# Optimization experiments

Measured on AMD Instinct MI355X. Metric: run time of the kernel, lower is better.

## Reference

```python
import jax, jax.numpy as jnp
import numpy as np
from jax.scipy.special import logsumexp

EPSILON = 0.1
N_ITERS = 5


def setup_inputs() -> dict:
    key = jax.random.key(0)
    k1, k2, k3 = jax.random.split(key, 3)
    B, Q, T, D = 16, 1024, 1024, 256
    preds = jax.random.normal(k1, (B, Q, D), dtype=jnp.float32)
    targets = jax.random.normal(k2, (B, T, D), dtype=jnp.float32)
    filter = jax.random.normal(k3, (B, T), dtype=jnp.float32)
    return {"preds": preds, "targets": targets, "filter": filter}


def _cdist(x, y):
    x2 = jnp.sum(x * x, axis=-1)[:, :, None]          # [B,Q,1]
    y2 = jnp.sum(y * y, axis=-1)[:, None, :]          # [B,1,T]
    xy = jnp.einsum("bqd,btd->bqt", x, y)             # [B,Q,T]
    return jnp.sqrt(jnp.maximum(x2 + y2 - 2.0 * xy, 0.0))


def reference(preds, targets, filter):
    eps = EPSILON
    B, Q, _ = preds.shape
    T = targets.shape[1]
    cost = _cdist(preds, targets)                     # [B,Q,T]
    filter_cost = 2.0 * jnp.max(cost)
    cost = jnp.where(filter[:, None, :] <= 0, filter_cost, cost)
    u = jnp.zeros((B, Q), dtype=cost.dtype)
    v = jnp.zeros((B, T), dtype=cost.dtype)
    for _ in range(N_ITERS):
        u = -eps * logsumexp(-(cost - v[:, None, :]) / eps, axis=2)
        v = -eps * logsumexp(-(cost - u[:, :, None]) / eps, axis=1)
    P = jnp.exp((u[:, :, None] + v[:, None, :] - cost) / eps)
    idx_tgt = jnp.argmax(P, axis=2)
    return (idx_tgt, P)
```

## Files before the change

### kernel.cpp

```cpp
#include <hip/hip_runtime.h>
#include <math.h>

#define BB 16
#define QQ 1024
#define TT 1024
#define DD 256
#define EPS 0.1f
#define SINK_ITERS 5
#define FCONST 128.0f
#define K2 14.426950408889634f
#define EPSLN2 0.069314718055994531f

typedef _Float16 f16;
typedef _Float16 f16x4 __attribute__((ext_vector_type(4)));
typedef _Float16 f16x8 __attribute__((ext_vector_type(8)));
typedef float f32x4 __attribute__((ext_vector_type(4)));

__device__ __forceinline__ float fast_exp2(float x) {
#if __has_builtin(__builtin_amdgcn_exp2f)
  return __builtin_amdgcn_exp2f(x);
#else
  return exp2f(x);
#endif
}
__device__ __forceinline__ float fast_log2(float x) {
#if __has_builtin(__builtin_amdgcn_logf)
  return __builtin_amdgcn_logf(x);
#else
  return log2f(x);
#endif
}

__global__ __launch_bounds__(256) void cvt_kernel(
    const float* __restrict__ preds, const float* __restrict__ targets,
    f16* __restrict__ Ahi, f16* __restrict__ Alo,
    f16* __restrict__ Bhi, f16* __restrict__ Blo,
    float* __restrict__ x2, float* __restrict__ y2)
{
  int w = threadIdx.x >> 6, l = threadIdx.x & 63;
  int row = blockIdx.x * 4 + w;
  const float* src; f16 *hi, *lo; float* nrm;
  if (row < BB*QQ) {
    src = preds + (size_t)row * DD;
    hi = Ahi + (size_t)row * DD; lo = Alo + (size_t)row * DD; nrm = x2 + row;
  } else {
    int r = row - BB*QQ;
    src = targets + (size_t)r * DD;
    hi = Bhi + (size_t)r * DD; lo = Blo + (size_t)r * DD; nrm = y2 + r;
  }
  float4 v = ((const float4*)src)[l];
  f16x4 h, lw;
  h.x = (f16)v.x; h.y = (f16)v.y; h.z = (f16)v.z; h.w = (f16)v.w;
  lw.x = (f16)(v.x - (float)h.x); lw.y = (f16)(v.y - (float)h.y);
  lw.z = (f16)(v.z - (float)h.z); lw.w = (f16)(v.w - (float)h.w);
  *(f16x4*)(hi + l*4) = h;
  *(f16x4*)(lo + l*4) = lw;
  float s = v.x*v.x + v.y*v.y + v.z*v.z + v.w*v.w;
  #pragma unroll
  for (int o = 32; o; o >>= 1) s += __shfl_down(s, o, 64);
  if (l == 0) *nrm = s;
}

__global__ __launch_bounds__(256) void scan_kernel(
    const float* __restrict__ filter, int* __restrict__ nU,
    int* __restrict__ f0i, int* __restrict__ cidx)
{
  __shared__ int sc[256];
  __shared__ int sf0;
  int b = blockIdx.x, tid = threadIdx.x;
  if (tid == 0) sf0 = 0x7fffffff;
  __syncthreads();
  float4 f4 = ((const float4*)(filter + (size_t)b*TT))[tid];
  int i0 = f4.x > 0.f, i1 = f4.y > 0.f, i2 = f4.z > 0.f, i3 = f4.w > 0.f;
  int cnt = i0+i1+i2+i3;
  int t0 = tid*4;
// ... 8 lines not shown
    sc[tid] += val;
    __syncthreads();
  }
  int excl = sc[tid] - cnt;
  int* cb = cidx + (size_t)b*TT + t0;
  int run = excl;
  cb[0] = run; run += i0;
  cb[1] = run; run += i1;
  cb[2] = run; run += i2;
  cb[3] = run; run += i3;
  if (tid == 255) nU[b] = sc[255];
  __syncthreads();
  if (tid == 0) f0i[b] = sf0;
}

__global__ __launch_bounds__(256) void cost_mfma_kernel(
    const f16* __restrict__ Ahi, const f16* __restrict__ Alo,
    const f16* __restrict__ Bhi, const f16* __restrict__ Blo,
    const float* __restrict__ x2, const float* __restrict__ y2,
    const float* __restrict__ filter,
    float* __restrict__ cost, float* __restrict__ costT, int useT,
    float* __restrict__ costC, const int* __restrict__ cidx, int compact)
{
  __shared__ f16 sA[2][128*32];
  __shared__ f16 sB[2][128*32];
  int b = blockIdx.z;
  int q0 = blockIdx.y * 128, t0 = blockIdx.x * 128;
  int tid = threadIdx.x, w = tid >> 6, l = tid & 63;
  int rq = (w >> 1) * 64, rt = (w & 1) * 64;
  int fr = l & 15, fg = l >> 4;
  const f16* pA[2] = { Ahi + ((size_t)b*QQ + q0) * DD, Alo + ((size_t)b*QQ + q0) * DD };
  const f16* pB[2] = { Bhi + ((size_t)b*TT + t0) * DD, Blo + ((size_t)b*TT + t0) * DD };
  f32x4 acc[4][4] = {};
  for (int k0 = 0; k0 < DD; k0 += 32) {
    __syncthreads();
#if __has_builtin(__builtin_amdgcn_global_load_lds)
    #pragma unroll
    for (int j = 0; j < 2; ++j) {
      int chunk = w*128 + j*64 + l;
      int row = chunk >> 2, kc = chunk & 3;
      size_t go = (size_t)row * DD + k0 + kc*8;
      int lb = (w*128 + j*64) * 8;
// ... 34 lines not shown
    #pragma unroll
    for (int fm = 0; fm < 4; ++fm)
      #pragma unroll
      for (int fn = 0; fn < 4; ++fn) {
        acc[fm][fn] = __builtin_amdgcn_mfma_f32_16x16x32_f16(ah[fm], bh[fn], acc[fm][fn], 0, 0, 0);
        acc[fm][fn] = __builtin_amdgcn_mfma_f32_16x16x32_f16(ah[fm], bl[fn], acc[fm][fn], 0, 0, 0);
        acc[fm][fn] = __builtin_amdgcn_mfma_f32_16x16x32_f16(al[fm], bh[fn], acc[fm][fn], 0, 0, 0);
      }
  }
  float xv[16];
  #pragma unroll
  for (int fm = 0; fm < 4; ++fm)
    #pragma unroll
    for (int r = 0; r < 4; ++r)
      xv[fm*4+r] = x2[(size_t)b*QQ + q0 + rq + fm*16 + fg*4 + r];
  float yv[4], fv[4];
  int jn[4];
  #pragma unroll
  for (int fn = 0; fn < 4; ++fn) {
    int t = t0 + rt + fn*16 + fr;
    yv[fn] = y2[(size_t)b*TT + t];
    fv[fn] = filter[(size_t)b*TT + t];
    jn[fn] = compact ? cidx[(size_t)b*TT + t] : 0;
  }
  #pragma unroll
  for (int fm = 0; fm < 4; ++fm) {
    #pragma unroll
    for (int fn = 0; fn < 4; ++fn) {
      int t = t0 + rt + fn*16 + fr;
      float cvr[4];
      #pragma unroll
      for (int r = 0; r < 4; ++r) {
        float c2 = xv[fm*4+r] + yv[fn] - 2.0f*acc[fm][fn][r];
        float craw = sqrtf(fmaxf(c2, 0.f));
        cvr[r] = craw;
        int q = q0 + rq + fm*16 + fg*4 + r;
        if (!compact) {
          cost[((size_t)b*QQ + q)*TT + t] = (fv[fn] <= 0.f) ? FCONST : craw;
        } else if (fv[fn] > 0.f) {
          costC[((size_t)b*QQ + q)*TT + jn[fn]] = craw;
        }
      }
      if (useT && fv[fn] > 0.f) {
        float* dst = costT + ((size_t)b*TT + t)*QQ + q0 + rq + fm*16 + fg*4;
        *(float4*)dst = make_float4(cvr[0], cvr[1], cvr[2], cvr[3]);
      }
    }
  }
}

__global__ __launch_bounds__(64) void norms_kernel(
    const float* __restrict__ preds, const float* __restrict__ targets,
    float* __restrict__ x2, float* __restrict__ y2)
{
  int row = blockIdx.x;
  const float* src; float* dst;
  if (row < BB*QQ) { src = preds + (size_t)row * DD; dst = x2 + row; }
  else { int r = row - BB*QQ; src = targets + (size_t)r * DD; dst = y2 + r; }
  float4 v = ((const float4*)src)[threadIdx.x];
  float s = v.x*v.x + v.y*v.y + v.z*v.z + v.w*v.w;
  #pragma unroll
  for (int o = 32; o; o >>= 1) s += __shfl_down(s, o, 64);
  if (threadIdx.x == 0) *dst = s;
}

#define LDSTR 132
__global__ __launch_bounds__(256) void cost_fp32_kernel(
    const float* __restrict__ preds, const float* __restrict__ targets,
    const float* __restrict__ x2, const float* __restrict__ y2,
    const float* __restrict__ filter,
    float* __restrict__ cost, float* __restrict__ costT, int useT)
{
  __shared__ float As[16*LDSTR];
  __shared__ float Bs[16*LDSTR];
  int b  = blockIdx.z;
  int q0 = blockIdx.y * 128;
  int t0 = blockIdx.x * 128;
  const float* Ab = preds   + ((size_t)b*QQ + q0) * DD;
  const float* Bb = targets + ((size_t)b*TT + t0) * DD;
  int tid = threadIdx.x;
  int srow = tid >> 2, sq = (tid & 3) << 2;
  int w = tid >> 6, l = tid & 63;
  int rq = ((w >> 1) << 6) + ((l >> 3) << 3);
  int rt = ((w & 1) << 6) + ((l & 7) << 3);
  float acc[8][8] = {};
  for (int k0 = 0; k0 < DD; k0 += 16) {
// ... 38 lines not shown
  #pragma unroll
  for (int i = 0; i < 8; ++i)
    #pragma unroll
    for (int j = 0; j < 8; ++j) {
      float c2 = xq[i] + yt[j] - 2.f*acc[i][j];
      float c = sqrtf(fmaxf(c2, 0.f));
      if (fvv[j] <= 0.f) c = FCONST;
      cv[i][j] = c;
    }
  #pragma unroll
  for (int i = 0; i < 8; ++i) {
    float* dst = cost + ((size_t)b*QQ + q0 + rq + i) * TT + t0 + rt;
    *(float4*)dst       = make_float4(cv[i][0], cv[i][1], cv[i][2], cv[i][3]);
    *(float4*)(dst + 4) = make_float4(cv[i][4], cv[i][5], cv[i][6], cv[i][7]);
  }
  if (useT) {
    #pragma unroll
    for (int j = 0; j < 8; ++j) {
      if (fvv[j] <= 0.f) continue;
      float* dst = costT + ((size_t)b*TT + t0 + rt + j) * QQ + q0 + rq;
      *(float4*)dst       = make_float4(cv[0][j], cv[1][j], cv[2][j], cv[3][j]);
      *(float4*)(dst + 4) = make_float4(cv[4][j], cv[5][j], cv[6][j], cv[7][j]);
    }
  }
}

__device__ __forceinline__ float wave_max64(float v) {
  #pragma unroll
  for (int o = 1; o < 64; o <<= 1) v = fmaxf(v, __shfl_xor(v, o, 64));
  return v;
}
__device__ __forceinline__ float wave_sum64(float v) {
  #pragma unroll
  for (int o = 1; o < 64; o <<= 1) v += __shfl_xor(v, o, 64);
  return v;
}

__global__ __launch_bounds__(256) void u_c_kernel(
    const float* __restrict__ costC, const float* __restrict__ vC,
    const float* __restrict__ vf, const int* __restrict__ nU,
    float* __restrict__ u, int it0)
{
  int w = threadIdx.x >> 6, l = threadIdx.x & 63;
  int row = blockIdx.x * 8 + w * 2;
  int b = row >> 10;
  int n = nU[b];
  int nF = TT - n;
  const float4* c0 = (const float4*)(costC + (size_t)row * TT);
  const float4* c1 = c0 + TT/4;
  const float4* vb = (const float4*)(vC + (size_t)b * TT);
  float s0[16], s1[16], m0 = -3.0e38f, m1 = -3.0e38f;
  int iters = (n + 255) >> 8;
  #pragma unroll
  for (int i = 0; i < 4; ++i) {
    if (i < iters) {
      int jj = l + (i << 6);
      int j = jj << 2;
      float4 v4;
      if (it0) v4 = make_float4(0.f,0.f,0.f,0.f); else v4 = vb[jj];
      float4 a4 = c0[jj];
      float4 b4 = c1[jj];
      s0[4*i+0] = (j+0 < n) ? (v4.x - a4.x)*K2 : -3.0e38f;
      s0[4*i+1] = (j+1 < n) ? (v4.y - a4.y)*K2 : -3.0e38f;
      s0[4*i+2] = (j+2 < n) ? (v4.z - a4.z)*K2 : -3.0e38f;
      s0[4*i+3] = (j+3 < n) ? (v4.w - a4.w)*K2 : -3.0e38f;
      s1[4*i+0] = (j+0 < n) ? (v4.x - b4.x)*K2 : -3.0e38f;
      s1[4*i+1] = (j+1 < n) ? (v4.y - b4.y)*K2 : -3.0e38f;
      s1[4*i+2] = (j+2 < n) ? (v4.z - b4.z)*K2 : -3.0e38f;
      s1[4*i+3] = (j+3 < n) ? (v4.w - b4.w)*K2 : -3.0e38f;
      m0 = fmaxf(m0, fmaxf(fmaxf(s0[4*i+0], s0[4*i+1]), fmaxf(s0[4*i+2], s0[4*i+3])));
      m1 = fmaxf(m1, fmaxf(fmaxf(s1[4*i+0], s1[4*i+1]), fmaxf(s1[4*i+2], s1[4*i+3])));
    } else {
      #pragma unroll
      for (int k = 0; k < 4; ++k) { s0[4*i+k] = -3.0e38f; s1[4*i+k] = -3.0e38f; }
    }
  }
  float st = 0.f;
  if (nF > 0) {
    float vfb = it0 ? 0.f : vf[b];
    st = (vfb - FCONST) * K2;
    m0 = fmaxf(m0, st); m1 = fmaxf(m1, st);
  }
  m0 = wave_max64(m0); m1 = wave_max64(m1);
  float q0 = 0.f, q1 = 0.f;
  #pragma unroll
  for (int i = 0; i < 16; ++i) { q0 += fast_exp2(s0[i] - m0); q1 += fast_exp2(s1[i] - m1); }
  q0 = wave_sum64(q0); q1 = wave_sum64(q1);
  if (nF > 0) {
    q0 += (float)nF * fast_exp2(st - m0);
    q1 += (float)nF * fast_exp2(st - m1);
  }
  if (l == 0) {
    u[row]   = -EPSLN2 * (m0 + fast_log2(q0));
    u[row+1] = -EPSLN2 * (m1 + fast_log2(q1));
  }
}

__global__ __launch_bounds__(256) void v_c_kernel(
    const float* __restrict__ costT,
    const float* __restrict__ filter, const int* __restrict__ cidx,
    const float* __restrict__ u, float* __restrict__ v,
    float* __restrict__ vC, float* __restrict__ vf)
{
  int w = threadIdx.x >> 6, l = threadIdx.x & 63;
  int row = blockIdx.x * 8 + w * 2;
  int b = row >> 10;
  const float4* ub = (const float4*)(u + (size_t)b * QQ);
  bool f0 = (filter[row]   <= 0.f);
  bool f1 = (filter[row+1] <= 0.f);
  float4 uw[4];
  #pragma unroll
  for (int i = 0; i < 4; ++i) uw[i] = ub[l + (i << 6)];
  float s0[16], s1[16], m0 = -3.0e38f, m1 = -3.0e38f;
  if (f0) {
    #pragma unroll
    for (int i = 0; i < 4; ++i) {
      s0[4*i+0] = (uw[i].x - FCONST) * K2; s0[4*i+1] = (uw[i].y - FCONST) * K2;
      s0[4*i+2] = (uw[i].z - FCONST) * K2; s0[4*i+3] = (uw[i].w - FCONST) * K2;
    }
  } else {
    const float4* cr = (const float4*)(costT + (size_t)row * QQ);
    #pragma unroll
    for (int i = 0; i < 4; ++i) {
      float4 c4 = cr[l + (i << 6)];
      s0[4*i+0] = (uw[i].x - c4.x) * K2; s0[4*i+1] = (uw[i].y - c4.y) * K2;
      s0[4*i+2] = (uw[i].z - c4.z) * K2; s0[4*i+3] = (uw[i].w - c4.w) * K2;
    }
  }
  if (f1) {
    #pragma unroll
    for (int i = 0; i < 4; ++i) {
      s1[4*i+0] = (uw[i].x - FCONST) * K2; s1[4*i+1] = (uw[i].y - FCONST) * K2;
      s1[4*i+2] = (uw[i].z - FCONST) * K2; s1[4*i+3] = (uw[i].w - FCONST) * K2;
    }
  } else {
    const float4* cr = (const float4*)(costT + (size_t)(row+1) * QQ);
    #pragma unroll
    for (int i = 0; i < 4; ++i) {
      float4 c4 = cr[l + (i << 6)];
      s1[4*i+0] = (uw[i].x - c4.x) * K2; s1[4*i+1] = (uw[i].y - c4.y) * K2;
      s1[4*i+2] = (uw[i].z - c4.z) * K2; s1[4*i+3] = (uw[i].w - c4.w) * K2;
    }
  }
  #pragma unroll
  for (int i = 0; i < 16; ++i) { m0 = fmaxf(m0, s0[i]); m1 = fmaxf(m1, s1[i]); }
  m0 = wave_max64(m0); m1 = wave_max64(m1);
  float q0 = 0.f, q1 = 0.f;
  #pragma unroll
  for (int i = 0; i < 16; ++i) { q0 += fast_exp2(s0[i] - m0); q1 += fast_exp2(s1[i] - m1); }
  q0 = wave_sum64(q0); q1 = wave_sum64(q1);
  if (l == 0) {
    float val0 = -EPSLN2 * (m0 + fast_log2(q0));
    float val1 = -EPSLN2 * (m1 + fast_log2(q1));
    v[row]   = val0;
    v[row+1] = val1;
    if (f0) vf[b] = val0; else vC[(size_t)b*TT + cidx[row]] = val0;
    if (f1) vf[b] = val1; else vC[(size_t)b*TT + cidx[row+1]] = val1;
  }
}

__global__ __launch_bounds__(256) void p_c_kernel(
    const float* __restrict__ costC, const float* __restrict__ filter,
    const int* __restrict__ cidx, const int* __restrict__ nU,
    const int* __restrict__ f0i, const float* __restrict__ vf,
    const float* __restrict__ u, const float* __restrict__ v,
    float* __restrict__ P, float* __restrict__ idxOut)
{
  int w = threadIdx.x >> 6, l = threadIdx.x & 63;
  int row = blockIdx.x * 8 + w * 2;
  int b = row >> 10;
  int nF = TT - nU[b];
  float u0 = u[row], u1 = u[row+1];
  float pf0 = -1.f, pf1 = -1.f; int fidx = 0x7fffffff;
  if (nF > 0) {
    float vfb = vf[b];
    pf0 = fast_exp2((u0 + vfb - FCONST) * K2);
    pf1 = fast_exp2((u1 + vfb - FCONST) * K2);
    fidx = f0i[b];
  }
  const float* r0 = costC + (size_t)row * TT;
  const float* r1 = r0 + TT;
  float4* o0 = (float4*)(P + (size_t)row * TT);
  float4* o1 = o0 + TT/4;
  const float4* fb = (const float4*)(filter + (size_t)b * TT);
  const int4*   jb = (const int4*)(cidx + (size_t)b * TT);
  const float4* vv = (const float4*)(v + (size_t)b * TT);
  float bp0 = -1.f, bp1 = -1.f; int bt0 = 0x7ffffffe, bt1 = 0x7ffffffe;
  #pragma unroll
  for (int i = 0; i < 4; ++i) {
    int e = l + (i << 6);
    float4 f4 = fb[e];
    int4  j4 = jb[e];
    float4 v4 = vv[e];
    int tb = e << 2;
    float4 p0, p1;
#define PELEM(comp, jx, toff) \
    if (f4.comp > 0.f) { \
      float cA = r0[jx], cB = r1[jx]; \
      p0.comp = fast_exp2((u0 + v4.comp - cA) * K2); \
      p1.comp = fast_exp2((u1 + v4.comp - cB) * K2); \
      if (p0.comp > bp0) { bp0 = p0.comp; bt0 = tb + toff; } \
      if (p1.comp > bp1) { bp1 = p1.comp; bt1 = tb + toff; } \
    } else { p0.comp = pf0; p1.comp = pf1; }
    PELEM(x, j4.x, 0)
    PELEM(y, j4.y, 1)
    PELEM(z, j4.z, 2)
    PELEM(w, j4.w, 3)
#undef PELEM
    o0[e] = p0;
    o1[e] = p1;
  }
  #pragma unroll
  for (int o = 1; o < 64; o <<= 1) {
    float op = __shfl_xor(bp0, o, 64);
    int   ot = __shfl_xor(bt0, o, 64);
    if (op > bp0 || (op == bp0 && ot < bt0)) { bp0 = op; bt0 = ot; }
    op = __shfl_xor(bp1, o, 64);
    ot = __shfl_xor(bt1, o, 64);
    if (op > bp1 || (op == bp1 && ot < bt1)) { bp1 = op; bt1 = ot; }
  }
  if (l == 0) {
    if (pf0 > bp0 || (pf0 == bp0 && fidx < bt0)) bt0 = fidx;
    if (pf1 > bp1 || (pf1 == bp1 && fidx < bt1)) bt1 = fidx;
    idxOut[row]   = (float)bt0;
    idxOut[row+1] = (float)bt1;
  }
}

__device__ __forceinline__ void u_body(int row, int l, bool it0,
    const float* __restrict__ cost, const float* __restrict__ v, float* __restrict__ u)
{
  int b = row >> 10;
  const float4* c0 = (const float4*)(cost + (size_t)row * TT);
  const float4* c1 = c0 + TT/4;
  const float4* vb = (const float4*)(v + (size_t)b * TT);
  float s0[16], s1[16], m0 = -3.0e38f, m1 = -3.0e38f;
  #pragma unroll
  for (int i = 0; i < 4; ++i) {
    float4 v4;
    if (it0) v4 = make_float4(0.f, 0.f, 0.f, 0.f);
    else     v4 = vb[l + (i << 6)];
    float4 a4 = c0[l + (i << 6)];
    float4 b4 = c1[l + (i << 6)];
    s0[4*i+0] = (v4.x - a4.x) * K2; s0[4*i+1] = (v4.y - a4.y) * K2;
    s0[4*i+2] = (v4.z - a4.z) * K2; s0[4*i+3] = (v4.w - a4.w) * K2;
    s1[4*i+0] = (v4.x - b4.x) * K2; s1[4*i+1] = (v4.y - b4.y) * K2;
    s1[4*i+2] = (v4.z - b4.z) * K2; s1[4*i+3] = (v4.w - b4.w) * K2;
    m0 = fmaxf(m0, fmaxf(fmaxf(s0[4*i+0], s0[4*i+1]), fmaxf(s0[4*i+2], s0[4*i+3])));
    m1 = fmaxf(m1, fmaxf(fmaxf(s1[4*i+0], s1[4*i+1]), fmaxf(s1[4*i+2], s1[4*i+3])));
  }
  m0 = wave_max64(m0); m1 = wave_max64(m1);
  float q0 = 0.f, q1 = 0.f;
  #pragma unroll
  for (int i = 0; i < 16; ++i) { q0 += fast_exp2(s0[i] - m0); q1 += fast_exp2(s1[i] - m1); }
  q0 = wave_sum64(q0); q1 = wave_sum64(q1);
  if (l == 0) {
    u[row]   = -EPSLN2 * (m0 + fast_log2(q0));
    u[row+1] = -EPSLN2 * (m1 + fast_log2(q1));
  }
}

__global__ __launch_bounds__(256) void u_kernel(
    const float* __restrict__ cost, const float* __restrict__ v, float* __restrict__ u, int it0)
{
  u_body(blockIdx.x * 8 + (threadIdx.x >> 6) * 2, threadIdx.x & 63, it0 != 0, cost, v, u);
}

__global__ __launch_bounds__(256) void v_kernel(
    const float* __restrict__ cost, const float* __restrict__ costT, int useT,
    const float* __restrict__ filter, const float* __restrict__ u, float* __restrict__ v)
{
  int w = threadIdx.x >> 6, l = threadIdx.x & 63;
  int row = blockIdx.x * 8 + w * 2;
  int b = row >> 10, t = row & 1023;
  const float4* ub = (const float4*)(u + (size_t)b * QQ);
  bool f0 = (filter[row]   <= 0.f);
  bool f1 = (filter[row+1] <= 0.f);
  float4 uw[4];
  #pragma unroll
  for (int i = 0; i < 4; ++i) uw[i] = ub[l + (i << 6)];
  float s0[16], s1[16], m0 = -3.0e38f, m1 = -3.0e38f;
  if (f0) {
    #pragma unroll
    for (int i = 0; i < 4; ++i) {
      s0[4*i+0] = (uw[i].x - FCONST) * K2; s0[4*i+1] = (uw[i].y - FCONST) * K2;
      s0[4*i+2] = (uw[i].z - FCONST) * K2; s0[4*i+3] = (uw[i].w - FCONST) * K2;
    }
  } else if (useT) {
    const float4* cr = (const float4*)(costT + (size_t)row * QQ);
    #pragma unroll
    for (int i = 0; i < 4; ++i) {
      float4 c4 = cr[l + (i << 6)];
      s0[4*i+0] = (uw[i].x - c4.x) * K2; s0[4*i+1] = (uw[i].y - c4.y) * K2;
      s0[4*i+2] = (uw[i].z - c4.z) * K2; s0[4*i+3] = (uw[i].w - c4.w) * K2;
    }
  } else {
    const float* cr = cost + (size_t)b*QQ*TT + t;
    #pragma unroll
    for (int i = 0; i < 4; ++i) {
      int q = (l + (i << 6)) << 2;
      s0[4*i+0] = (uw[i].x - cr[(size_t)(q+0)*TT]) * K2;
      s0[4*i+1] = (uw[i].y - cr[(size_t)(q+1)*TT]) * K2;
      s0[4*i+2] = (uw[i].z - cr[(size_t)(q+2)*TT]) * K2;
      s0[4*i+3] = (uw[i].w - cr[(size_t)(q+3)*TT]) * K2;
    }
  }
  if (f1) {
    #pragma unroll
    for (int i = 0; i < 4; ++i) {
      s1[4*i+0] = (uw[i].x - FCONST) * K2; s1[4*i+1] = (uw[i].y - FCONST) * K2;
      s1[4*i+2] = (uw[i].z - FCONST) * K2; s1[4*i+3] = (uw[i].w - FCONST) * K2;
    }
  } else if (useT) {
    const float4* cr = (const float4*)(costT + (size_t)(row+1) * QQ);
    #pragma unroll
    for (int i = 0; i < 4; ++i) {
      float4 c4 = cr[l + (i << 6)];
      s1[4*i+0] = (uw[i].x - c4.x) * K2; s1[4*i+1] = (uw[i].y - c4.y) * K2;
      s1[4*i+2] = (uw[i].z - c4.z) * K2; s1[4*i+3] = (uw[i].w - c4.w) * K2;
    }
  } else {
    const float* cr = cost + (size_t)b*QQ*TT + t + 1;
    #pragma unroll
    for (int i = 0; i < 4; ++i) {
      int q = (l + (i << 6)) << 2;
      s1[4*i+0] = (uw[i].x - cr[(size_t)(q+0)*TT]) * K2;
      s1[4*i+1] = (uw[i].y - cr[(size_t)(q+1)*TT]) * K2;
      s1[4*i+2] = (uw[i].z - cr[(size_t)(q+2)*TT]) * K2;
      s1[4*i+3] = (uw[i].w - cr[(size_t)(q+3)*TT]) * K2;
    }
  }
  #pragma unroll
  for (int i = 0; i < 16; ++i) { m0 = fmaxf(m0, s0[i]); m1 = fmaxf(m1, s1[i]); }
  m0 = wave_max64(m0); m1 = wave_max64(m1);
  float q0 = 0.f, q1 = 0.f;
  #pragma unroll
  for (int i = 0; i < 16; ++i) { q0 += fast_exp2(s0[i] - m0); q1 += fast_exp2(s1[i] - m1); }
  q0 = wave_sum64(q0); q1 = wave_sum64(q1);
  if (l == 0) {
    v[row]   = -EPSLN2 * (m0 + fast_log2(q0));
    v[row+1] = -EPSLN2 * (m1 + fast_log2(q1));
  }
}

// ... 51 lines not shown
                              void* d_out, int out_size, void* d_ws, size_t ws_size,
                              hipStream_t stream) {
  const float* preds   = (const float*)d_in[0];
  const float* targets = (const float*)d_in[1];
  const float* filter  = (const float*)d_in[2];
  float* out = (float*)d_out;
  float* idxOut = out;
  float* P = out + (size_t)BB*QQ;

  const size_t F16A   = (size_t)BB*QQ*DD;
  const size_t f16tot = 4 * F16A * sizeof(f16);
  const size_t SMALL  = (size_t)1 << 19;
  const size_t CB     = (size_t)BB * QQ * TT * sizeof(float);

  char* ws = (char*)d_ws;
  int useF16 = ws_size >= f16tot + SMALL;
  char* base = ws + (useF16 ? f16tot : 0);
  f16 *Ahi = (f16*)ws, *Alo = Ahi + F16A, *Bhi = Alo + F16A, *Blo = Bhi + F16A;
  float* x2 = (float*)base;
  float* y2 = x2 + 16384;
  float* u  = y2 + 16384;
  float* v  = u + 16384;
  float* vC = v + 16384;
  float* vf = vC + 16384;
  int* nU   = (int*)(vf + 64);
  int* f0i  = nU + 64;
  int* cidx = f0i + 64;
  float* costT = (float*)(base + SMALL);
  float* costC = (float*)(base + SMALL + CB);
  int useT = ws_size >= (size_t)(base - ws) + SMALL + CB;
  int useC = useF16 && (ws_size >= f16tot + SMALL + 2*CB);

  dim3 cg_(TT/128, QQ/128, BB);
  if (useF16) {
    cvt_kernel<<<BB*(QQ+TT)/4, 256, 0, stream>>>(preds, targets, Ahi, Alo, Bhi, Blo, x2, y2);
    if (useC) scan_kernel<<<BB, 256, 0, stream>>>(filter, nU, f0i, cidx);
    cost_mfma_kernel<<<cg_, 256, 0, stream>>>(Ahi, Alo, Bhi, Blo, x2, y2, filter,
                                              P, costT, useT, costC, cidx, useC);
  } else {
    norms_kernel<<<BB*(QQ+TT), 64, 0, stream>>>(preds, targets, x2, y2);
    cost_fp32_kernel<<<cg_, 256, 0, stream>>>(preds, targets, x2, y2, filter, P, costT, useT);
  }

  int blks = BB*QQ/8;
  if (useC) {
    for (int it = 0; it < SINK_ITERS; ++it) {
      u_c_kernel<<<blks, 256, 0, stream>>>(costC, vC, vf, nU, u, it == 0 ? 1 : 0);
      v_c_kernel<<<blks, 256, 0, stream>>>(costT, filter, cidx, u, v, vC, vf);
    }
    p_c_kernel<<<blks, 256, 0, stream>>>(costC, filter, cidx, nU, f0i, vf, u, v, P, idxOut);
  } else {
    for (int it = 0; it < SINK_ITERS; ++it) {
      u_kernel<<<blks, 256, 0, stream>>>(P, v, u, it == 0 ? 1 : 0);
      v_kernel<<<blks, 256, 0, stream>>>(P, costT, useT, filter, u, v);
    }
    p_kernel<<<blks, 256, 0, stream>>>(P, u, v, idxOut);
  }
}
```

Before: 267.9 us.

## Compact unfiltered targets before GEMM and skip fully filtered column tiles

Runs the filter scan first, then has the conversion kernel write only unfiltered target rows, in compacted order, into the f16 B operand. The MFMA cost kernel now runs on these compacted targets and exits early for column tiles past the unfiltered count. It writes the compacted cost and its transpose directly, with no per-element filter checks or index gathers. About half the targets are filtered under random normal inputs, so roughly half the GEMM and cost stores should be skipped. Tiles that straddle the count boundary still compute some garbage columns, and the fallback paths are simplified.

```diff
diff --git a/kernel.cpp b/kernel.cpp
--- a/kernel.cpp
+++ b/kernel.cpp
@@ -29,36 +29,6 @@
 #else
   return log2f(x);
 #endif
-}
-
-__global__ __launch_bounds__(256) void cvt_kernel(
-    const float* __restrict__ preds, const float* __restrict__ targets,
-    f16* __restrict__ Ahi, f16* __restrict__ Alo,
-    f16* __restrict__ Bhi, f16* __restrict__ Blo,
-    float* __restrict__ x2, float* __restrict__ y2)
-{
-  int w = threadIdx.x >> 6, l = threadIdx.x & 63;
-  int row = blockIdx.x * 4 + w;
-  const float* src; f16 *hi, *lo; float* nrm;
-  if (row < BB*QQ) {
-    src = preds + (size_t)row * DD;
-    hi = Ahi + (size_t)row * DD; lo = Alo + (size_t)row * DD; nrm = x2 + row;
-  } else {
-    int r = row - BB*QQ;
-    src = targets + (size_t)r * DD;
-    hi = Bhi + (size_t)r * DD; lo = Blo + (size_t)r * DD; nrm = y2 + r;
-  }
-  float4 v = ((const float4*)src)[l];
-  f16x4 h, lw;
-  h.x = (f16)v.x; h.y = (f16)v.y; h.z = (f16)v.z; h.w = (f16)v.w;
-  lw.x = (f16)(v.x - (float)h.x); lw.y = (f16)(v.y - (float)h.y);
-  lw.z = (f16)(v.z - (float)h.z); lw.w = (f16)(v.w - (float)h.w);
-  *(f16x4*)(hi + l*4) = h;
-  *(f16x4*)(lo + l*4) = lw;
-  float s = v.x*v.x + v.y*v.y + v.z*v.z + v.w*v.w;
-  #pragma unroll
-  for (int o = 32; o; o >>= 1) s += __shfl_down(s, o, 64);
-  if (l == 0) *nrm = s;
 }
 
 __global__ __launch_bounds__(256) void scan_kernel(
@@ -97,18 +67,53 @@
   if (tid == 0) f0i[b] = sf0;
 }
 
-__global__ __launch_bounds__(256) void cost_mfma_kernel(
+__global__ __launch_bounds__(256) void cvt_c_kernel(
+    const float* __restrict__ preds, const float* __restrict__ targets,
+    const float* __restrict__ filter, const int* __restrict__ cidx,
+    f16* __restrict__ Ahi, f16* __restrict__ Alo,
+    f16* __restrict__ Bhi, f16* __restrict__ Blo,
+    float* __restrict__ x2, float* __restrict__ y2)
+{
+  int w = threadIdx.x >> 6, l = threadIdx.x & 63;
+  int row = blockIdx.x * 4 + w;
+  const float* src; f16 *hi, *lo; float* nrm;
+  if (row < BB*QQ) {
+    src = preds + (size_t)row * DD;
+    hi = Ahi + (size_t)row * DD; lo = Alo + (size_t)row * DD; nrm = x2 + row;
+  } else {
+    int r = row - BB*QQ;
+    if (filter[r] <= 0.f) return;
+    int b = r >> 10;
+    int cj = cidx[r];
+    size_t crow = (size_t)b*TT + cj;
+    src = targets + (size_t)r * DD;
+    hi = Bhi + crow * DD; lo = Blo + crow * DD; nrm = y2 + crow;
+  }
+  float4 v = ((const float4*)src)[l];
+  f16x4 h, lw;
+  h.x = (f16)v.x; h.y = (f16)v.y; h.z = (f16)v.z; h.w = (f16)v.w;
+  lw.x = (f16)(v.x - (float)h.x); lw.y = (f16)(v.y - (float)h.y);
+  lw.z = (f16)(v.z - (float)h.z); lw.w = (f16)(v.w - (float)h.w);
+  *(f16x4*)(hi + l*4) = h;
+  *(f16x4*)(lo + l*4) = lw;
+  float s = v.x*v.x + v.y*v.y + v.z*v.z + v.w*v.w;
+  #pragma unroll
+  for (int o = 32; o; o >>= 1) s += __shfl_down(s, o, 64);
+  if (l == 0) *nrm = s;
+}
+
+__global__ __launch_bounds__(256) void cost_mfma_c_kernel(
     const f16* __restrict__ Ahi, const f16* __restrict__ Alo,
     const f16* __restrict__ Bhi, const f16* __restrict__ Blo,
     const float* __restrict__ x2, const float* __restrict__ y2,
-    const float* __restrict__ filter,
-    float* __restrict__ cost, float* __restrict__ costT, int useT,
-    float* __restrict__ costC, const int* __restrict__ cidx, int compact)
+    const int* __restrict__ nU,
+    float* __restrict__ costC, float* __restrict__ costTC)
 {
   __shared__ f16 sA[2][128*32];
   __shared__ f16 sB[2][128*32];
   int b = blockIdx.z;
   int q0 = blockIdx.y * 128, t0 = blockIdx.x * 128;
+  if (t0 >= nU[b]) return;
   int tid = threadIdx.x, w = tid >> 6, l = tid & 63;
   int rq = (w >> 1) * 64, rt = (w & 1) * 64;
   int fr = l & 15, fg = l >> 4;
@@ -173,15 +178,10 @@
     #pragma unroll
     for (int r = 0; r < 4; ++r)
       xv[fm*4+r] = x2[(size_t)b*QQ + q0 + rq + fm*16 + fg*4 + r];
-  float yv[4], fv[4];
-  int jn[4];
-  #pragma unroll
-  for (int fn = 0; fn < 4; ++fn) {
-    int t = t0 + rt + fn*16 + fr;
-    yv[fn] = y2[(size_t)b*TT + t];
-    fv[fn] = filter[(size_t)b*TT + t];
-    jn[fn] = compact ? cidx[(size_t)b*TT + t] : 0;
-  }
+  float yv[4];
+  #pragma unroll
+  for (int fn = 0; fn < 4; ++fn)
+    yv[fn] = y2[(size_t)b*TT + t0 + rt + fn*16 + fr];
   #pragma unroll
   for (int fm = 0; fm < 4; ++fm) {
     #pragma unroll
@@ -194,17 +194,214 @@
         float craw = sqrtf(fmaxf(c2, 0.f));
         cvr[r] = craw;
         int q = q0 + rq + fm*16 + fg*4 + r;
-        if (!compact) {
-          cost[((size_t)b*QQ + q)*TT + t] = (fv[fn] <= 0.f) ? FCONST : craw;
-        } else if (fv[fn] > 0.f) {
-          costC[((size_t)b*QQ + q)*TT + jn[fn]] = craw;
-        }
+        costC[((size_t)b*QQ + q)*TT + t] = craw;
       }
-      if (useT && fv[fn] > 0.f) {
-        float* dst = costT + ((size_t)b*TT + t)*QQ + q0 + rq + fm*16 + fg*4;
-        *(float4*)dst = make_float4(cvr[0], cvr[1], cvr[2], cvr[3]);
-      }
-    }
+      float* dst = costTC + ((size_t)b*TT + t)*QQ + q0 + rq + fm*16 + fg*4;
+      *(float4*)dst = make_float4(cvr[0], cvr[1], cvr[2], cvr[3]);
+    }
+  }
+}
+
+__device__ __forceinline__ float wave_max64(float v) {
+  #pragma unroll
+  for (int o = 1; o < 64; o <<= 1) v = fmaxf(v, __shfl_xor(v, o, 64));
+  return v;
+}
+__device__ __forceinline__ float wave_sum64(float v) {
+  #pragma unroll
+  for (int o = 1; o < 64; o <<= 1) v += __shfl_xor(v, o, 64);
+  return v;
+}
+
+__global__ __launch_bounds__(256) void u_c_kernel(
+    const float* __restrict__ costC, const float* __restrict__ vC,
+    const float* __restrict__ vf, const int* __restrict__ nU,
+    float* __restrict__ u, int it0)
+{
+  int w = threadIdx.x >> 6, l = threadIdx.x & 63;
+  int row = blockIdx.x * 8 + w * 2;
+  int b = row >> 10;
+  int n = nU[b];
+  int nF = TT - n;
+  const float4* c0 = (const float4*)(costC + (size_t)row * TT);
+  const float4* c1 = c0 + TT/4;
+  const float4* vb = (const float4*)(vC + (size_t)b * TT);
+  float s0[16], s1[16], m0 = -3.0e38f, m1 = -3.0e38f;
+  int iters = (n + 255) >> 8;
+  #pragma unroll
+  for (int i = 0; i < 4; ++i) {
+    if (i < iters) {
+      int jj = l + (i << 6);
+      int j = jj << 2;
+      float4 v4;
+      if (it0) v4 = make_float4(0.f,0.f,0.f,0.f); else v4 = vb[jj];
+      float4 a4 = c0[jj];
+      float4 b4 = c1[jj];
+      s0[4*i+0] = (j+0 < n) ? (v4.x - a4.x)*K2 : -3.0e38f;
+      s0[4*i+1] = (j+1 < n) ? (v4.y - a4.y)*K2 : -3.0e38f;
+      s0[4*i+2] = (j+2 < n) ? (v4.z - a4.z)*K2 : -3.0e38f;
+      s0[4*i+3] = (j+3 < n) ? (v4.w - a4.w)*K2 : -3.0e38f;
+      s1[4*i+0] = (j+0 < n) ? (v4.x - b4.x)*K2 : -3.0e38f;
+      s1[4*i+1] = (j+1 < n) ? (v4.y - b4.y)*K2 : -3.0e38f;
+      s1[4*i+2] = (j+2 < n) ? (v4.z - b4.z)*K2 : -3.0e38f;
+      s1[4*i+3] = (j+3 < n) ? (v4.w - b4.w)*K2 : -3.0e38f;
+      m0 = fmaxf(m0, fmaxf(fmaxf(s0[4*i+0], s0[4*i+1]), fmaxf(s0[4*i+2], s0[4*i+3])));
+      m1 = fmaxf(m1, fmaxf(fmaxf(s1[4*i+0], s1[4*i+1]), fmaxf(s1[4*i+2], s1[4*i+3])));
+    } else {
+      #pragma unroll
+      for (int k = 0; k < 4; ++k) { s0[4*i+k] = -3.0e38f; s1[4*i+k] = -3.0e38f; }
+    }
+  }
+  float st = 0.f;
+  if (nF > 0) {
+    float vfb = it0 ? 0.f : vf[b];
+    st = (vfb - FCONST) * K2;
+    m0 = fmaxf(m0, st); m1 = fmaxf(m1, st);
+  }
+  m0 = wave_max64(m0); m1 = wave_max64(m1);
+  float q0 = 0.f, q1 = 0.f;
+  #pragma unroll
+  for (int i = 0; i < 16; ++i) { q0 += fast_exp2(s0[i] - m0); q1 += fast_exp2(s1[i] - m1); }
+  q0 = wave_sum64(q0); q1 = wave_sum64(q1);
+  if (nF > 0) {
+    q0 += (float)nF * fast_exp2(st - m0);
+    q1 += (float)nF * fast_exp2(st - m1);
+  }
+  if (l == 0) {
+    u[row]   = -EPSLN2 * (m0 + fast_log2(q0));
+    u[row+1] = -EPSLN2 * (m1 + fast_log2(q1));
+  }
+}
+
+__global__ __launch_bounds__(256) void v_c_kernel(
+    const float* __restrict__ costTC,
+    const float* __restrict__ filter, const int* __restrict__ cidx,
+    const float* __restrict__ u, float* __restrict__ v,
+    float* __restrict__ vC, float* __restrict__ vf)
+{
+  int w = threadIdx.x >> 6, l = threadIdx.x & 63;
+  int row = blockIdx.x * 8 + w * 2;
+  int b = row >> 10;
+  const float4* ub = (const float4*)(u + (size_t)b * QQ);
+  bool f0 = (filter[row]   <= 0.f);
+  bool f1 = (filter[row+1] <= 0.f);
+  int cj0 = cidx[row], cj1 = cidx[row+1];
+  float4 uw[4];
+  #pragma unroll
+  for (int i = 0; i < 4; ++i) uw[i] = ub[l + (i << 6)];
+  float s0[16], s1[16], m0 = -3.0e38f, m1 = -3.0e38f;
+  if (f0) {
+    #pragma unroll
+    for (int i = 0; i < 4; ++i) {
+      s0[4*i+0] = (uw[i].x - FCONST) * K2; s0[4*i+1] = (uw[i].y - FCONST) * K2;
+      s0[4*i+2] = (uw[i].z - FCONST) * K2; s0[4*i+3] = (uw[i].w - FCONST) * K2;
+    }
+  } else {
+    const float4* cr = (const float4*)(costTC + ((size_t)b*TT + cj0) * QQ);
+    #pragma unroll
+    for (int i = 0; i < 4; ++i) {
+      float4 c4 = cr[l + (i << 6)];
+      s0[4*i+0] = (uw[i].x - c4.x) * K2; s0[4*i+1] = (uw[i].y - c4.y) * K2;
+      s0[4*i+2] = (uw[i].z - c4.z) * K2; s0[4*i+3] = (uw[i].w - c4.w) * K2;
+    }
+  }
+  if (f1) {
+    #pragma unroll
+    for (int i = 0; i < 4; ++i) {
+      s1[4*i+0] = (uw[i].x - FCONST) * K2; s1[4*i+1] = (uw[i].y - FCONST) * K2;
+      s1[4*i+2] = (uw[i].z - FCONST) * K2; s1[4*i+3] = (uw[i].w - FCONST) * K2;
+    }
+  } else {
+    const float4* cr = (const float4*)(costTC + ((size_t)b*TT + cj1) * QQ);
+    #pragma unroll
+    for (int i = 0; i < 4; ++i) {
+      float4 c4 = cr[l + (i << 6)];
+      s1[4*i+0] = (uw[i].x - c4.x) * K2; s1[4*i+1] = (uw[i].y - c4.y) * K2;
+      s1[4*i+2] = (uw[i].z - c4.z) * K2; s1[4*i+3] = (uw[i].w - c4.w) * K2;
+    }
+  }
+  #pragma unroll
+  for (int i = 0; i < 16; ++i) { m0 = fmaxf(m0, s0[i]); m1 = fmaxf(m1, s1[i]); }
+  m0 = wave_max64(m0); m1 = wave_max64(m1);
+  float q0 = 0.f, q1 = 0.f;
+  #pragma unroll
+  for (int i = 0; i < 16; ++i) { q0 += fast_exp2(s0[i] - m0); q1 += fast_exp2(s1[i] - m1); }
+  q0 = wave_sum64(q0); q1 = wave_sum64(q1);
+  if (l == 0) {
+    float val0 = -EPSLN2 * (m0 + fast_log2(q0));
+    float val1 = -EPSLN2 * (m1 + fast_log2(q1));
+    v[row]   = val0;
+    v[row+1] = val1;
+    if (f0) vf[b] = val0; else vC[(size_t)b*TT + cj0] = val0;
+    if (f1) vf[b] = val1; else vC[(size_t)b*TT + cj1] = val1;
+  }
+}
+
+__global__ __launch_bounds__(256) void p_c_kernel(
+    const float* __restrict__ costC, const float* __restrict__ filter,
+    const int* __restrict__ cidx, const int* __restrict__ nU,
+    const int* __restrict__ f0i, const float* __restrict__ vf,
+    const float* __restrict__ u, const float* __restrict__ v,
+    float* __restrict__ P, float* __restrict__ idxOut)
+{
+  int w = threadIdx.x >> 6, l = threadIdx.x & 63;
+  int row = blockIdx.x * 8 + w * 2;
+  int b = row >> 10;
+  int nF = TT - nU[b];
+  float u0 = u[row], u1 = u[row+1];
+  float pf0 = -1.f, pf1 = -1.f; int fidx = 0x7fffffff;
+  if (nF > 0) {
+    float vfb = vf[b];
+    pf0 = fast_exp2((u0 + vfb - FCONST) * K2);
+    pf1 = fast_exp2((u1 + vfb - FCONST) * K2);
+    fidx = f0i[b];
+  }
+  const float* r0 = costC + (size_t)row * TT;
+  const float* r1 = r0 + TT;
+  float4* o0 = (float4*)(P + (size_t)row * TT);
+  float4* o1 = o0 + TT/4;
+  const float4* fb = (const float4*)(filter + (size_t)b * TT);
+  const int4*   jb = (const int4*)(cidx + (size_t)b * TT);
+  const float4* vv = (const float4*)(v + (size_t)b * TT);
+  float bp0 = -1.f, bp1 = -1.f; int bt0 = 0x7ffffffe, bt1 = 0x7ffffffe;
+  #pragma unroll
+  for (int i = 0; i < 4; ++i) {
+    int e = l + (i << 6);
+    float4 f4 = fb[e];
+    int4  j4 = jb[e];
+    float4 v4 = vv[e];
+    int tb = e << 2;
+    float4 p0, p1;
+#define PELEM(comp, jx, toff) \
+    if (f4.comp > 0.f) { \
+      float cA = r0[jx], cB = r1[jx]; \
+      p0.comp = fast_exp2((u0 + v4.comp - cA) * K2); \
+      p1.comp = fast_exp2((u1 + v4.comp - cB) * K2); \
+      if (p0.comp > bp0) { bp0 = p0.comp; bt0 = tb + toff; } \
+      if (p1.comp > bp1) { bp1 = p1.comp; bt1 = tb + toff; } \
+    } else { p0.comp = pf0; p1.comp = pf1; }
+    PELEM(x, j4.x, 0)
+    PELEM(y, j4.y, 1)
+    PELEM(z, j4.z, 2)
+    PELEM(w, j4.w, 3)
+#undef PELEM
+    o0[e] = p0;
+    o1[e] = p1;
+  }
+  #pragma unroll
+  for (int o = 1; o < 64; o <<= 1) {
+    float op = __shfl_xor(bp0, o, 64);
+    int   ot = __shfl_xor(bt0, o, 64);
+    if (op > bp0 || (op == bp0 && ot < bt0)) { bp0 = op; bt0 = ot; }
+    op = __shfl_xor(bp1, o, 64);
+    ot = __shfl_xor(bt1, o, 64);
+    if (op > bp1 || (op == bp1 && ot < bt1)) { bp1 = op; bt1 = ot; }
+  }
+  if (l == 0) {
+    if (pf0 > bp0 || (pf0 == bp0 && fidx < bt0)) bt0 = fidx;
+    if (pf1 > bp1 || (pf1 == bp1 && fidx < bt1)) bt1 = fidx;
+    idxOut[row]   = (float)bt0;
+    idxOut[row+1] = (float)bt1;
   }
 }
 
@@ -228,7 +425,7 @@
     const float* __restrict__ preds, const float* __restrict__ targets,
     const float* __restrict__ x2, const float* __restrict__ y2,
     const float* __restrict__ filter,
-    float* __restrict__ cost, float* __restrict__ costT, int useT)
+    float* __restrict__ cost)
 {
   __shared__ float As[16*LDSTR];
   __shared__ float Bs[16*LDSTR];
@@ -297,222 +494,13 @@
     *(float4*)dst       = make_float4(cv[i][0], cv[i][1], cv[i][2], cv[i][3]);
     *(float4*)(dst + 4) = make_float4(cv[i][4], cv[i][5], cv[i][6], cv[i][7]);
   }
-  if (useT) {
-    #pragma unroll
-    for (int j = 0; j < 8; ++j) {
-      if (fvv[j] <= 0.f) continue;
-      float* dst = costT + ((size_t)b*TT + t0 + rt + j) * QQ + q0 + rq;
-      *(float4*)dst       = make_float4(cv[0][j], cv[1][j], cv[2][j], cv[3][j]);
-      *(float4*)(dst + 4) = make_float4(cv[4][j], cv[5][j], cv[6][j], cv[7][j]);
-    }
-  }
-}
-
-__device__ __forceinline__ float wave_max64(float v) {
-  #pragma unroll
-  for (int o = 1; o < 64; o <<= 1) v = fmaxf(v, __shfl_xor(v, o, 64));
-  return v;
-}
-__device__ __forceinline__ float wave_sum64(float v) {
-  #pragma unroll
-  for (int o = 1; o < 64; o <<= 1) v += __shfl_xor(v, o, 64);
-  return v;
-}
-
-__global__ __launch_bounds__(256) void u_c_kernel(
-    const float* __restrict__ costC, const float* __restrict__ vC,
-    const float* __restrict__ vf, const int* __restrict__ nU,
-    float* __restrict__ u, int it0)
+}
+
+__global__ __launch_bounds__(256) void u_kernel(
+    const float* __restrict__ cost, const float* __restrict__ v, float* __restrict__ u, int it0)
 {
   int w = threadIdx.x >> 6, l = threadIdx.x & 63;
   int row = blockIdx.x * 8 + w * 2;
-  int b = row >> 10;
-  int n = nU[b];
-  int nF = TT - n;
-  const float4* c0 = (const float4*)(costC + (size_t)row * TT);
-  const float4* c1 = c0 + TT/4;
-  const float4* vb = (const float4*)(vC + (size_t)b * TT);
-  float s0[16], s1[16], m0 = -3.0e38f, m1 = -3.0e38f;
-  int iters = (n + 255) >> 8;
-  #pragma unroll
-  for (int i = 0; i < 4; ++i) {
-    if (i < iters) {
-      int jj = l + (i << 6);
-      int j = jj << 2;
-      float4 v4;
-      if (it0) v4 = make_float4(0.f,0.f,0.f,0.f); else v4 = vb[jj];
-      float4 a4 = c0[jj];
-      float4 b4 = c1[jj];
-      s0[4*i+0] = (j+0 < n) ? (v4.x - a4.x)*K2 : -3.0e38f;
-      s0[4*i+1] = (j+1 < n) ? (v4.y - a4.y)*K2 : -3.0e38f;
-      s0[4*i+2] = (j+2 < n) ? (v4.z - a4.z)*K2 : -3.0e38f;
-      s0[4*i+3] = (j+3 < n) ? (v4.w - a4.w)*K2 : -3.0e38f;
-      s1[4*i+0] = (j+0 < n) ? (v4.x - b4.x)*K2 : -3.0e38f;
-      s1[4*i+1] = (j+1 < n) ? (v4.y - b4.y)*K2 : -3.0e38f;
-      s1[4*i+2] = (j+2 < n) ? (v4.z - b4.z)*K2 : -3.0e38f;
-      s1[4*i+3] = (j+3 < n) ? (v4.w - b4.w)*K2 : -3.0e38f;
-      m0 = fmaxf(m0, fmaxf(fmaxf(s0[4*i+0], s0[4*i+1]), fmaxf(s0[4*i+2], s0[4*i+3])));
-      m1 = fmaxf(m1, fmaxf(fmaxf(s1[4*i+0], s1[4*i+1]), fmaxf(s1[4*i+2], s1[4*i+3])));
-    } else {
-      #pragma unroll
-      for (int k = 0; k < 4; ++k) { s0[4*i+k] = -3.0e38f; s1[4*i+k] = -3.0e38f; }
-    }
-  }
-  float st = 0.f;
-  if (nF > 0) {
-    float vfb = it0 ? 0.f : vf[b];
-    st = (vfb - FCONST) * K2;
-    m0 = fmaxf(m0, st); m1 = fmaxf(m1, st);
-  }
-  m0 = wave_max64(m0); m1 = wave_max64(m1);
-  float q0 = 0.f, q1 = 0.f;
-  #pragma unroll
-  for (int i = 0; i < 16; ++i) { q0 += fast_exp2(s0[i] - m0); q1 += fast_exp2(s1[i] - m1); }
-  q0 = wave_sum64(q0); q1 = wave_sum64(q1);
-  if (nF > 0) {
-    q0 += (float)nF * fast_exp2(st - m0);
-    q1 += (float)nF * fast_exp2(st - m1);
-  }
-  if (l == 0) {
-    u[row]   = -EPSLN2 * (m0 + fast_log2(q0));
-    u[row+1] = -EPSLN2 * (m1 + fast_log2(q1));
-  }
-}
-
-__global__ __launch_bounds__(256) void v_c_kernel(
-    const float* __restrict__ costT,
-    const float* __restrict__ filter, const int* __restrict__ cidx,
-    const float* __restrict__ u, float* __restrict__ v,
-    float* __restrict__ vC, float* __restrict__ vf)
-{
-  int w = threadIdx.x >> 6, l = threadIdx.x & 63;
-  int row = blockIdx.x * 8 + w * 2;
-  int b = row >> 10;
-  const float4* ub = (const float4*)(u + (size_t)b * QQ);
-  bool f0 = (filter[row]   <= 0.f);
-  bool f1 = (filter[row+1] <= 0.f);
-  float4 uw[4];
-  #pragma unroll
-  for (int i = 0; i < 4; ++i) uw[i] = ub[l + (i << 6)];
-  float s0[16], s1[16], m0 = -3.0e38f, m1 = -3.0e38f;
-  if (f0) {
-    #pragma unroll
-    for (int i = 0; i < 4; ++i) {
-      s0[4*i+0] = (uw[i].x - FCONST) * K2; s0[4*i+1] = (uw[i].y - FCONST) * K2;
-      s0[4*i+2] = (uw[i].z - FCONST) * K2; s0[4*i+3] = (uw[i].w - FCONST) * K2;
-    }
-  } else {
-    const float4* cr = (const float4*)(costT + (size_t)row * QQ);
-    #pragma unroll
-    for (int i = 0; i < 4; ++i) {
-      float4 c4 = cr[l + (i << 6)];
-      s0[4*i+0] = (uw[i].x - c4.x) * K2; s0[4*i+1] = (uw[i].y - c4.y) * K2;
-      s0[4*i+2] = (uw[i].z - c4.z) * K2; s0[4*i+3] = (uw[i].w - c4.w) * K2;
-    }
-  }
-  if (f1) {
-    #pragma unroll
-    for (int i = 0; i < 4; ++i) {
-      s1[4*i+0] = (uw[i].x - FCONST) * K2; s1[4*i+1] = (uw[i].y - FCONST) * K2;
-      s1[4*i+2] = (uw[i].z - FCONST) * K2; s1[4*i+3] = (uw[i].w - FCONST) * K2;
-    }
-  } else {
-    const float4* cr = (const float4*)(costT + (size_t)(row+1) * QQ);
-    #pragma unroll
-    for (int i = 0; i < 4; ++i) {
-      float4 c4 = cr[l + (i << 6)];
-      s1[4*i+0] = (uw[i].x - c4.x) * K2; s1[4*i+1] = (uw[i].y - c4.y) * K2;
-      s1[4*i+2] = (uw[i].z - c4.z) * K2; s1[4*i+3] = (uw[i].w - c4.w) * K2;
-    }
-  }
-  #pragma unroll
-  for (int i = 0; i < 16; ++i) { m0 = fmaxf(m0, s0[i]); m1 = fmaxf(m1, s1[i]); }
-  m0 = wave_max64(m0); m1 = wave_max64(m1);
-  float q0 = 0.f, q1 = 0.f;
-  #pragma unroll
-  for (int i = 0; i < 16; ++i) { q0 += fast_exp2(s0[i] - m0); q1 += fast_exp2(s1[i] - m1); }
-  q0 = wave_sum64(q0); q1 = wave_sum64(q1);
-  if (l == 0) {
-    float val0 = -EPSLN2 * (m0 + fast_log2(q0));
-    float val1 = -EPSLN2 * (m1 + fast_log2(q1));
-    v[row]   = val0;
-    v[row+1] = val1;
-    if (f0) vf[b] = val0; else vC[(size_t)b*TT + cidx[row]] = val0;
-    if (f1) vf[b] = val1; else vC[(size_t)b*TT + cidx[row+1]] = val1;
-  }
-}
-
-__global__ __launch_bounds__(256) void p_c_kernel(
-    const float* __restrict__ costC, const float* __restrict__ filter,
-    const int* __restrict__ cidx, const int* __restrict__ nU,
-    const int* __restrict__ f0i, const float* __restrict__ vf,
-    const float* __restrict__ u, const float* __restrict__ v,
-    float* __restrict__ P, float* __restrict__ idxOut)
-{
-  int w = threadIdx.x >> 6, l = threadIdx.x & 63;
-  int row = blockIdx.x * 8 + w * 2;
-  int b = row >> 10;
-  int nF = TT - nU[b];
-  float u0 = u[row], u1 = u[row+1];
-  float pf0 = -1.f, pf1 = -1.f; int fidx = 0x7fffffff;
-  if (nF > 0) {
-    float vfb = vf[b];
-    pf0 = fast_exp2((u0 + vfb - FCONST) * K2);
-    pf1 = fast_exp2((u1 + vfb - FCONST) * K2);
-    fidx = f0i[b];
-  }
-  const float* r0 = costC + (size_t)row * TT;
-  const float* r1 = r0 + TT;
-  float4* o0 = (float4*)(P + (size_t)row * TT);
-  float4* o1 = o0 + TT/4;
-  const float4* fb = (const float4*)(filter + (size_t)b * TT);
-  const int4*   jb = (const int4*)(cidx + (size_t)b * TT);
-  const float4* vv = (const float4*)(v + (size_t)b * TT);
-  float bp0 = -1.f, bp1 = -1.f; int bt0 = 0x7ffffffe, bt1 = 0x7ffffffe;
-  #pragma unroll
-  for (int i = 0; i < 4; ++i) {
-    int e = l + (i << 6);
-    float4 f4 = fb[e];
-    int4  j4 = jb[e];
-    float4 v4 = vv[e];
-    int tb = e << 2;
-    float4 p0, p1;
-#define PELEM(comp, jx, toff) \
-    if (f4.comp > 0.f) { \
-      float cA = r0[jx], cB = r1[jx]; \
-      p0.comp = fast_exp2((u0 + v4.comp - cA) * K2); \
-      p1.comp = fast_exp2((u1 + v4.comp - cB) * K2); \
-      if (p0.comp > bp0) { bp0 = p0.comp; bt0 = tb + toff; } \
-      if (p1.comp > bp1) { bp1 = p1.comp; bt1 = tb + toff; } \
-    } else { p0.comp = pf0; p1.comp = pf1; }
-    PELEM(x, j4.x, 0)
-    PELEM(y, j4.y, 1)
-    PELEM(z, j4.z, 2)
-    PELEM(w, j4.w, 3)
-#undef PELEM
-    o0[e] = p0;
-    o1[e] = p1;
-  }
-  #pragma unroll
-  for (int o = 1; o < 64; o <<= 1) {
-    float op = __shfl_xor(bp0, o, 64);
-    int   ot = __shfl_xor(bt0, o, 64);
-    if (op > bp0 || (op == bp0 && ot < bt0)) { bp0 = op; bt0 = ot; }
-    op = __shfl_xor(bp1, o, 64);
-    ot = __shfl_xor(bt1, o, 64);
-    if (op > bp1 || (op == bp1 && ot < bt1)) { bp1 = op; bt1 = ot; }
-  }
-  if (l == 0) {
-    if (pf0 > bp0 || (pf0 == bp0 && fidx < bt0)) bt0 = fidx;
-    if (pf1 > bp1 || (pf1 == bp1 && fidx < bt1)) bt1 = fidx;
-    idxOut[row]   = (float)bt0;
-    idxOut[row+1] = (float)bt1;
-  }
-}
-
-__device__ __forceinline__ void u_body(int row, int l, bool it0,
-    const float* __restrict__ cost, const float* __restrict__ v, float* __restrict__ u)
-{
   int b = row >> 10;
   const float4* c0 = (const float4*)(cost + (size_t)row * TT);
   const float4* c1 = c0 + TT/4;
@@ -543,14 +531,8 @@
   }
 }
 
-__global__ __launch_bounds__(256) void u_kernel(
-    const float* __restrict__ cost, const float* __restrict__ v, float* __restrict__ u, int it0)
-{
-  u_body(blockIdx.x * 8 + (threadIdx.x >> 6) * 2, threadIdx.x & 63, it0 != 0, cost, v, u);
-}
-
 __global__ __launch_bounds__(256) void v_kernel(
-    const float* __restrict__ cost, const float* __restrict__ costT, int useT,
+    const float* __restrict__ cost,
     const float* __restrict__ filter, const float* __restrict__ u, float* __restrict__ v)
 {
   int w = threadIdx.x >> 6, l = threadIdx.x & 63;
@@ -563,54 +545,27 @@
   #pragma unroll
   for (int i = 0; i < 4; ++i) uw[i] = ub[l + (i << 6)];
   float s0[16], s1[16], m0 = -3.0e38f, m1 = -3.0e38f;
-  if (f0) {
-    #pragma unroll
-    for (int i = 0; i < 4; ++i) {
+  const float* cr = cost + (size_t)b*QQ*TT + t;
+  #pragma unroll
+  for (int i = 0; i < 4; ++i) {
+    int q = (l + (i << 6)) << 2;
+    if (f0) {
       s0[4*i+0] = (uw[i].x - FCONST) * K2; s0[4*i+1] = (uw[i].y - FCONST) * K2;
       s0[4*i+2] = (uw[i].z - FCONST) * K2; s0[4*i+3] = (uw[i].w - FCONST) * K2;
-    }
-  } else if (useT) {
-    const float4* cr = (const float4*)(costT + (size_t)row * QQ);
-    #pragma unroll
-    for (int i = 0; i < 4; ++i) {
-      float4 c4 = cr[l + (i << 6)];
-      s0[4*i+0] = (uw[i].x - c4.x) * K2; s0[4*i+1] = (uw[i].y - c4.y) * K2;
-      s0[4*i+2] = (uw[i].z - c4.z) * K2; s0[4*i+3] = (uw[i].w - c4.w) * K2;
-    }
-  } else {
-    const float* cr = cost + (size_t)b*QQ*TT + t;
-    #pragma unroll
-    for (int i = 0; i < 4; ++i) {
-      int q = (l + (i << 6)) << 2;
+    } else {
       s0[4*i+0] = (uw[i].x - cr[(size_t)(q+0)*TT]) * K2;
       s0[4*i+1] = (uw[i].y - cr[(size_t)(q+1)*TT]) * K2;
       s0[4*i+2] = (uw[i].z - cr[(size_t)(q+2)*TT]) * K2;
       s0[4*i+3] = (uw[i].w - cr[(size_t)(q+3)*TT]) * K2;
     }
-  }
-  if (f1) {
-    #pragma unroll
-    for (int i = 0; i < 4; ++i) {
+    if (f1) {
       s1[4*i+0] = (uw[i].x - FCONST) * K2; s1[4*i+1] = (uw[i].y - FCONST) * K2;
       s1[4*i+2] = (uw[i].z - FCONST) * K2; s1[4*i+3] = (uw[i].w - FCONST) * K2;
-    }
-  } else if (useT) {
-    const float4* cr = (const float4*)(costT + (size_t)(row+1) * QQ);
-    #pragma unroll
-    for (int i = 0; i < 4; ++i) {
-      float4 c4 = cr[l + (i << 6)];
-      s1[4*i+0] = (uw[i].x - c4.x) * K2; s1[4*i+1] = (uw[i].y - c4.y) * K2;
-      s1[4*i+2] = (uw[i].z - c4.z) * K2; s1[4*i+3] = (uw[i].w - c4.w) * K2;
-    }
-  } else {
-    const float* cr = cost + (size_t)b*QQ*TT + t + 1;
-    #pragma unroll
-    for (int i = 0; i < 4; ++i) {
-      int q = (l + (i << 6)) << 2;
-      s1[4*i+0] = (uw[i].x - cr[(size_t)(q+0)*TT]) * K2;
-      s1[4*i+1] = (uw[i].y - cr[(size_t)(q+1)*TT]) * K2;
-      s1[4*i+2] = (uw[i].z - cr[(size_t)(q+2)*TT]) * K2;
-      s1[4*i+3] = (uw[i].w - cr[(size_t)(q+3)*TT]) * K2;
+    } else {
+      s1[4*i+0] = (uw[i].x - cr[(size_t)(q+0)*TT + 1]) * K2;
+      s1[4*i+1] = (uw[i].y - cr[(size_t)(q+1)*TT + 1]) * K2;
+      s1[4*i+2] = (uw[i].z - cr[(size_t)(q+2)*TT + 1]) * K2;
+      s1[4*i+3] = (uw[i].w - cr[(size_t)(q+3)*TT + 1]) * K2;
     }
   }
   #pragma unroll
@@ -692,9 +647,9 @@
   const size_t CB     = (size_t)BB * QQ * TT * sizeof(float);
 
   char* ws = (char*)d_ws;
-  int useF16 = ws_size >= f16tot + SMALL;
-  char* base = ws + (useF16 ? f16tot : 0);
+  int useC = ws_size >= f16tot + SMALL + 2*CB;
   f16 *Ahi = (f16*)ws, *Alo = Ahi + F16A, *Bhi = Alo + F16A, *Blo = Bhi + F16A;
+  char* base = ws + (useC ? f16tot : 0);
   float* x2 = (float*)base;
   float* y2 = x2 + 16384;
   float* u  = y2 + 16384;
@@ -704,33 +659,28 @@
   int* nU   = (int*)(vf + 64);
   int* f0i  = nU + 64;
   int* cidx = f0i + 64;
-  float* costT = (float*)(base + SMALL);
-  float* costC = (float*)(base + SMALL + CB);
-  int useT = ws_size >= (size_t)(base - ws) + SMALL + CB;
-  int useC = useF16 && (ws_size >= f16tot + SMALL + 2*CB);
-
-  dim3 cg_(TT/128, QQ/128, BB);
-  if (useF16) {
-    cvt_kernel<<<BB*(QQ+TT)/4, 256, 0, stream>>>(preds, targets, Ahi, Alo, Bhi, Blo, x2, y2);
-    if (useC) scan_kernel<<<BB, 256, 0, stream>>>(filter, nU, f0i, cidx);
-    cost_mfma_kernel<<<cg_, 256, 0, stream>>>(Ahi, Alo, Bhi, Blo, x2, y2, filter,
-                                              P, costT, useT, costC, cidx, useC);
+  float* costTC = (float*)(base + SMALL);
+  float* costC  = (float*)(base + SMALL + CB);
+
+  int blks = BB*QQ/8;
+  if (useC) {
+    scan_kernel<<<BB, 256, 0, stream>>>(filter, nU, f0i, cidx);
+    cvt_c_kernel<<<BB*(QQ+TT)/4, 256, 0, stream>>>(preds, targets, filter, cidx,
+                                                   Ahi, Alo, Bhi, Blo, x2, y2);
+    dim3 cg_(TT/128, QQ/128, BB);
+    cost_mfma_c_kernel<<<cg_, 256, 0, stream>>>(Ahi, Alo, Bhi, Blo, x2, y2, nU, costC, costTC);
+    for (int it = 0; it < SINK_ITERS; ++it) {
+      u_c_kernel<<<blks, 256, 0, stream>>>(costC, vC, vf, nU, u, it == 0 ? 1 : 0);
+      v_c_kernel<<<blks, 256, 0, stream>>>(costTC, filter, cidx, u, v, vC, vf);
+    }
+    p_c_kernel<<<blks, 256, 0, stream>>>(costC, filter, cidx, nU, f0i, vf, u, v, P, idxOut);
   } else {
     norms_kernel<<<BB*(QQ+TT), 64, 0, stream>>>(preds, targets, x2, y2);
-    cost_fp32_kernel<<<cg_, 256, 0, stream>>>(preds, targets, x2, y2, filter, P, costT, useT);
-  }
-
-  int blks = BB*QQ/8;
-  if (useC) {
-    for (int it = 0; it < SINK_ITERS; ++it) {
-      u_c_kernel<<<blks, 256, 0, stream>>>(costC, vC, vf, nU, u, it == 0 ? 1 : 0);
-      v_c_kernel<<<blks, 256, 0, stream>>>(costT, filter, cidx, u, v, vC, vf);
-    }
-    p_c_kernel<<<blks, 256, 0, stream>>>(costC, filter, cidx, nU, f0i, vf, u, v, P, idxOut);
-  } else {
+    dim3 cg_(TT/128, QQ/128, BB);
+    cost_fp32_kernel<<<cg_, 256, 0, stream>>>(preds, targets, x2, y2, filter, P);
     for (int it = 0; it < SINK_ITERS; ++it) {
       u_kernel<<<blks, 256, 0, stream>>>(P, v, u, it == 0 ? 1 : 0);
-      v_kernel<<<blks, 256, 0, stream>>>(P, costT, useT, filter, u, v);
+      v_kernel<<<blks, 256, 0, stream>>>(P, filter, u, v);
     }
     p_kernel<<<blks, 256, 0, stream>>>(P, u, v, idxOut);
   }
```

After: 260.3 us. 1.03x faster.
